# Optimization experiments

Hardware: AMD Instinct MI355X
Metric: run time of the kernel (lower is better)

Reference implementation:

```python
import jax, jax.numpy as jnp
import numpy as np

BS, NQ, NC, NT = 16, 900, 91, 1600
COST_CLASS, COST_BBOX, COST_GIOU = 1.0, 5.0, 2.0


def box_cxcywh_to_xyxy(b):
    cx, cy, w, h = b[..., 0], b[..., 1], b[..., 2], b[..., 3]
    return jnp.stack([cx - 0.5 * w, cy - 0.5 * h, cx + 0.5 * w, cy + 0.5 * h], axis=-1)


def generalized_box_iou(boxes1, boxes2):
    # boxes1: [N,4] xyxy, boxes2: [M,4] xyxy -> [N,M]
    area1 = (boxes1[:, 2] - boxes1[:, 0]) * (boxes1[:, 3] - boxes1[:, 1])  # [N]
    area2 = (boxes2[:, 2] - boxes2[:, 0]) * (boxes2[:, 3] - boxes2[:, 1])  # [M]
    lt = jnp.maximum(boxes1[:, None, :2], boxes2[None, :, :2])  # [N,M,2]
    rb = jnp.minimum(boxes1[:, None, 2:], boxes2[None, :, 2:])  # [N,M,2]
    wh = jnp.clip(rb - lt, 0.0)
    inter = wh[..., 0] * wh[..., 1]  # [N,M]
    union = area1[:, None] + area2[None, :] - inter
    iou = inter / union
    # smallest enclosing box
    lt_c = jnp.minimum(boxes1[:, None, :2], boxes2[None, :, :2])
    rb_c = jnp.maximum(boxes1[:, None, 2:], boxes2[None, :, 2:])
    wh_c = jnp.clip(rb_c - lt_c, 0.0)
    area_c = wh_c[..., 0] * wh_c[..., 1]
    return iou - (area_c - union) / area_c


def setup_inputs() -> dict:
    key = jax.random.key(0)
    k1, k2, k3, k4 = jax.random.split(key, 4)
    pred_logits = jax.random.normal(k1, (BS, NQ, NC), dtype=jnp.float32)
    # cxcywh in (0,1): guarantee positive w,h and sane boxes
    pred_boxes = jax.random.uniform(k2, (BS, NQ, 4), dtype=jnp.float32, minval=0.05, maxval=0.95)
    tgt_bbox = jax.random.uniform(k3, (NT, 4), dtype=jnp.float32, minval=0.05, maxval=0.95)
    tgt_ids = jax.random.randint(k4, (NT,), 0, NC, dtype=jnp.int32)
    return {"pred_logits": pred_logits, "pred_boxes": pred_boxes,
            "tgt_bbox": tgt_bbox, "tgt_ids": tgt_ids}


def reference(pred_logits, pred_boxes, tgt_bbox, tgt_ids):
    bs, num_queries = pred_logits.shape[:2]
    out_prob = jax.nn.softmax(pred_logits.reshape(-1, pred_logits.shape[-1]), axis=-1)  # [bs*nq, NC]
    out_bbox = pred_boxes.reshape(-1, 4)  # [bs*nq, 4]
    cost_class = -out_prob[:, tgt_ids]  # [bs*nq, NT]
    # L1 cdist
    cost_bbox = jnp.sum(jnp.abs(out_bbox[:, None, :] - tgt_bbox[None, :, :]), axis=-1)
    cost_giou = -generalized_box_iou(box_cxcywh_to_xyxy(out_bbox), box_cxcywh_to_xyxy(tgt_bbox))
    C = COST_BBOX * cost_bbox + COST_CLASS * cost_class + COST_GIOU * cost_giou
    return C.reshape(bs, num_queries, -1)
```

## Files before the change

### kernel.cpp

```cpp
#include <hip/hip_runtime.h>
#include <math.h>

#define BS_ 16
#define NQ_ 900
#define NC_ 91
#define NT_ 1600
#define NROWS_ (BS_ * NQ_)
#define TILE_R 4
#define NBLK (NROWS_ / TILE_R)

__global__ __launch_bounds__(256) void matcher_cost_kernel(
    const float* __restrict__ logits,
    const float* __restrict__ pboxes,
    const float4* __restrict__ tboxes,
    const int*   __restrict__ tids,
    float* __restrict__ out)
{
    const int base = blockIdx.x * TILE_R;
    const int tid  = threadIdx.x;
    const int lane = tid & 63;
    const int wave = tid >> 6;

    __shared__ __align__(16) float sprob_t[NC_ * TILE_R];

    {
        const float* lrow = logits + (size_t)(base + wave) * NC_;
        float v0 = lrow[lane];
        float v1 = (lane < NC_ - 64) ? lrow[64 + lane] : -INFINITY;
        float m = fmaxf(v0, v1);
        #pragma unroll
        for (int off = 32; off >= 1; off >>= 1)
            m = fmaxf(m, __shfl_xor(m, off, 64));
        float e0 = __expf(v0 - m);
        float e1 = (lane < NC_ - 64) ? __expf(v1 - m) : 0.0f;
        float s = e0 + e1;
        #pragma unroll
        for (int off = 32; off >= 1; off >>= 1)
            s += __shfl_xor(s, off, 64);
        const float inv_s = __builtin_amdgcn_rcpf(s);
        sprob_t[lane * TILE_R + wave] = e0 * inv_s;
        if (lane < NC_ - 64)
            sprob_t[(64 + lane) * TILE_R + wave] = e1 * inv_s;
    }
    __syncthreads();

    float qcx[TILE_R], qcy[TILE_R], qw[TILE_R], qh[TILE_R];
    float qx0[TILE_R], qy0[TILE_R], qx1[TILE_R], qy1[TILE_R], qarea[TILE_R];
    #pragma unroll
    for (int r = 0; r < TILE_R; ++r) {
        const float4 qb = *reinterpret_cast<const float4*>(pboxes + (size_t)(base + r) * 4);
        qcx[r] = qb.x; qcy[r] = qb.y; qw[r] = qb.z; qh[r] = qb.w;
        qx0[r] = fmaf(-0.5f, qb.z, qb.x);
        qy0[r] = fmaf(-0.5f, qb.w, qb.y);
        qx1[r] = fmaf( 0.5f, qb.z, qb.x);
        qy1[r] = fmaf( 0.5f, qb.w, qb.y);
        qarea[r] = qb.z * qb.w;
    }

    for (int j = tid; j < NT_; j += 256) {
        const float4 tb = tboxes[j];
        const int id = tids[j];

        const float tx0 = fmaf(-0.5f, tb.z, tb.x);
        const float ty0 = fmaf(-0.5f, tb.w, tb.y);
        const float tx1 = fmaf( 0.5f, tb.z, tb.x);
        const float ty1 = fmaf( 0.5f, tb.w, tb.y);
        const float tarea = tb.z * tb.w;

        const float4 p4 = *reinterpret_cast<const float4*>(&sprob_t[id * TILE_R]);
        const float p[TILE_R] = {p4.x, p4.y, p4.z, p4.w};

        #pragma unroll
        for (int r = 0; r < TILE_R; ++r) {
            const float cb = fabsf(qcx[r] - tb.x) + fabsf(qcy[r] - tb.y)
                           + fabsf(qw[r]  - tb.z) + fabsf(qh[r]  - tb.w);

            const float iw = fmaxf(fminf(qx1[r], tx1) - fmaxf(qx0[r], tx0), 0.0f);
            const float ih = fmaxf(fminf(qy1[r], ty1) - fmaxf(qy0[r], ty0), 0.0f);
            const float inter = iw * ih;
            const float uni   = qarea[r] + tarea - inter;

            const float cw = fmaxf(qx1[r], tx1) - fminf(qx0[r], tx0);
            const float ch = fmaxf(qy1[r], ty1) - fminf(qy0[r], ty0);
            const float areac = cw * ch;

            float c = fmaf(5.0f, cb, 2.0f - p[r]);
            c = fmaf(-2.0f * inter, __builtin_amdgcn_rcpf(uni),   c);
            c = fmaf(-2.0f * uni,   __builtin_amdgcn_rcpf(areac), c);

            __builtin_nontemporal_store(c, out + (size_t)(base + r) * NT_ + j);
        }
    }
}

extern "C" void kernel_launch(void* const* d_in, const int* in_sizes, int n_in,
                              void* d_out, int out_size, void* d_ws, size_t ws_size,
                              hipStream_t stream) {
    const float*  logits = (const float*)d_in[0];
    const float*  pboxes = (const float*)d_in[1];
    const float4* tboxes = (const float4*)d_in[2];
    const int*    tids   = (const int*)d_in[3];
    float* out = (float*)d_out;

    matcher_cost_kernel<<<NBLK, 256, 0, stream>>>(logits, pboxes, tboxes, tids, out);
}
```

Before: 120.0 us.

## Use 320-thread blocks with fully unrolled target loop and prefetched target boxes

Block size changes to 320 so each thread handles exactly 5 targets (1600/320) in a fully unrolled loop with no remainder. Target boxes and ids are loaded into registers before the barrier so their latency overlaps the softmax. The constant 2 is folded into the shared class term, and the enclosing-box width is computed algebraically from the intersection deltas, saving min/max ops. A fifth wave now idles during the softmax, and register pressure rises from holding the prefetched boxes.

```diff
diff --git a/kernel.cpp b/kernel.cpp
--- a/kernel.cpp
+++ b/kernel.cpp
@@ -7,9 +7,11 @@
 #define NT_ 1600
 #define NROWS_ (BS_ * NQ_)
 #define TILE_R 4
+#define TPB 320
 #define NBLK (NROWS_ / TILE_R)
+#define KITER (NT_ / TPB)
 
-__global__ __launch_bounds__(256) void matcher_cost_kernel(
+__global__ __launch_bounds__(TPB) void matcher_cost_kernel(
     const float* __restrict__ logits,
     const float* __restrict__ pboxes,
     const float4* __restrict__ tboxes,
@@ -21,10 +23,10 @@
     const int lane = tid & 63;
     const int wave = tid >> 6;
 
-    __shared__ __align__(16) float sprob_t[NC_ * TILE_R];
+    __shared__ __align__(16) float sneg[NC_ * TILE_R];
 
-    {
-        const float* lrow = logits + (size_t)(base + wave) * NC_;
+    if (wave < TILE_R) {
+        const float* lrow = logits + (base + wave) * NC_;
         float v0 = lrow[lane];
         float v1 = (lane < NC_ - 64) ? lrow[64 + lane] : -INFINITY;
         float m = fmaxf(v0, v1);
@@ -38,17 +40,25 @@
         for (int off = 32; off >= 1; off >>= 1)
             s += __shfl_xor(s, off, 64);
         const float inv_s = __builtin_amdgcn_rcpf(s);
-        sprob_t[lane * TILE_R + wave] = e0 * inv_s;
+        sneg[lane * TILE_R + wave] = fmaf(-e0, inv_s, 2.0f);
         if (lane < NC_ - 64)
-            sprob_t[(64 + lane) * TILE_R + wave] = e1 * inv_s;
+            sneg[(64 + lane) * TILE_R + wave] = fmaf(-e1, inv_s, 2.0f);
     }
-    __syncthreads();
+
+    float4 tb[KITER];
+    int    id[KITER];
+    #pragma unroll
+    for (int k = 0; k < KITER; ++k) {
+        const int j = k * TPB + tid;
+        tb[k] = tboxes[j];
+        id[k] = tids[j];
+    }
 
     float qcx[TILE_R], qcy[TILE_R], qw[TILE_R], qh[TILE_R];
     float qx0[TILE_R], qy0[TILE_R], qx1[TILE_R], qy1[TILE_R], qarea[TILE_R];
     #pragma unroll
     for (int r = 0; r < TILE_R; ++r) {
-        const float4 qb = *reinterpret_cast<const float4*>(pboxes + (size_t)(base + r) * 4);
+        const float4 qb = *reinterpret_cast<const float4*>(pboxes + (base + r) * 4);
         qcx[r] = qb.x; qcy[r] = qb.y; qw[r] = qb.z; qh[r] = qb.w;
         qx0[r] = fmaf(-0.5f, qb.z, qb.x);
         qy0[r] = fmaf(-0.5f, qb.w, qb.y);
@@ -57,38 +67,43 @@
         qarea[r] = qb.z * qb.w;
     }
 
-    for (int j = tid; j < NT_; j += 256) {
-        const float4 tb = tboxes[j];
-        const int id = tids[j];
+    __syncthreads();
 
-        const float tx0 = fmaf(-0.5f, tb.z, tb.x);
-        const float ty0 = fmaf(-0.5f, tb.w, tb.y);
-        const float tx1 = fmaf( 0.5f, tb.z, tb.x);
-        const float ty1 = fmaf( 0.5f, tb.w, tb.y);
-        const float tarea = tb.z * tb.w;
+    float4 pp[KITER];
+    #pragma unroll
+    for (int k = 0; k < KITER; ++k)
+        pp[k] = *reinterpret_cast<const float4*>(&sneg[id[k] * TILE_R]);
 
-        const float4 p4 = *reinterpret_cast<const float4*>(&sprob_t[id * TILE_R]);
-        const float p[TILE_R] = {p4.x, p4.y, p4.z, p4.w};
+    #pragma unroll
+    for (int k = 0; k < KITER; ++k) {
+        const int j = k * TPB + tid;
+        const float4 t = tb[k];
+        const float tx0 = fmaf(-0.5f, t.z, t.x);
+        const float ty0 = fmaf(-0.5f, t.w, t.y);
+        const float tx1 = fmaf( 0.5f, t.z, t.x);
+        const float ty1 = fmaf( 0.5f, t.w, t.y);
+        const float tarea = t.z * t.w;
+        const float p[TILE_R] = {pp[k].x, pp[k].y, pp[k].z, pp[k].w};
 
         #pragma unroll
         for (int r = 0; r < TILE_R; ++r) {
-            const float cb = fabsf(qcx[r] - tb.x) + fabsf(qcy[r] - tb.y)
-                           + fabsf(qw[r]  - tb.z) + fabsf(qh[r]  - tb.w);
+            const float cb = fabsf(qcx[r] - t.x) + fabsf(qcy[r] - t.y)
+                           + fabsf(qw[r]  - t.z) + fabsf(qh[r]  - t.w);
 
-            const float iw = fmaxf(fminf(qx1[r], tx1) - fmaxf(qx0[r], tx0), 0.0f);
-            const float ih = fmaxf(fminf(qy1[r], ty1) - fmaxf(qy0[r], ty0), 0.0f);
-            const float inter = iw * ih;
-            const float uni   = qarea[r] + tarea - inter;
+            const float dx = fminf(qx1[r], tx1) - fmaxf(qx0[r], tx0);
+            const float dy = fminf(qy1[r], ty1) - fmaxf(qy0[r], ty0);
+            const float inter = fmaxf(dx, 0.0f) * fmaxf(dy, 0.0f);
+            const float uni   = (qarea[r] + tarea) - inter;
 
-            const float cw = fmaxf(qx1[r], tx1) - fminf(qx0[r], tx0);
-            const float ch = fmaxf(qy1[r], ty1) - fminf(qy0[r], ty0);
+            const float cw = (qw[r] + t.z) - dx;
+            const float ch = (qh[r] + t.w) - dy;
             const float areac = cw * ch;
 
-            float c = fmaf(5.0f, cb, 2.0f - p[r]);
+            float c = fmaf(5.0f, cb, p[r]);
             c = fmaf(-2.0f * inter, __builtin_amdgcn_rcpf(uni),   c);
             c = fmaf(-2.0f * uni,   __builtin_amdgcn_rcpf(areac), c);
 
-            __builtin_nontemporal_store(c, out + (size_t)(base + r) * NT_ + j);
+            __builtin_nontemporal_store(c, out + (base + r) * NT_ + j);
         }
     }
 }
@@ -102,5 +117,5 @@
     const int*    tids   = (const int*)d_in[3];
     float* out = (float*)d_out;
 
-    matcher_cost_kernel<<<NBLK, 256, 0, stream>>>(logits, pboxes, tboxes, tids, out);
+    matcher_cost_kernel<<<NBLK, TPB, 0, stream>>>(logits, pboxes, tboxes, tids, out);
 }
```

After: 118.9 us. About the same (-0.9%).
